# Optimization experiments

Hardware: AMD Instinct MI355X
Metric: run time of the kernel (lower is better)

## Reference

```python
import jax, jax.numpy as jnp
import numpy as np

N = 200000      # nodes (1000 graphs x 200 nodes)
E = 1600000     # edges
N1 = 100000     # nodes after pool 1
E2 = 100000     # edges of pooled graph
N2 = 50000      # nodes after pool 2
B = 1000        # graphs
F_IN, C1, C2, H, NCLS = 1, 32, 64, 25, 10


def setup_inputs() -> dict:
    key = jax.random.key(0)
    ks = jax.random.split(key, 16)
    def lin(k, i, o):
        return jax.random.normal(k, (i, o), jnp.float32) / np.sqrt(i)
    inp = {
        'x': jax.random.normal(ks[0], (N, F_IN), jnp.float32),
        'pos': jax.random.uniform(ks[1], (N, 2), jnp.float32),
        'edge_index': jax.random.randint(ks[2], (2, E), 0, N, dtype=jnp.int32),
        'edge_attr': jax.random.uniform(ks[3], (E, 2), jnp.float32),
        'batch': (jnp.arange(N, dtype=jnp.int32) // (N // B)),
        'cluster1': (jnp.arange(N, dtype=jnp.int32) // 2),      # pairs of consecutive nodes -> same graph
        'edge_index2': jax.random.randint(ks[4], (2, E2), 0, N1, dtype=jnp.int32),
        'cluster2': (jnp.arange(N1, dtype=jnp.int32) // 2),
        'n1_w1': lin(ks[5], 2, H), 'n1_b1': jnp.zeros((H,), jnp.float32),
        'n1_w2': lin(ks[6], H, F_IN * C1), 'n1_b2': jnp.zeros((F_IN * C1,), jnp.float32),
        'root1': lin(ks[7], F_IN, C1), 'bias1': jnp.zeros((C1,), jnp.float32),
        'n2_w1': lin(ks[8], 2, H), 'n2_b1': jnp.zeros((H,), jnp.float32),
        'n2_w2': lin(ks[9], H, C1 * C2), 'n2_b2': jnp.zeros((C1 * C2,), jnp.float32),
        'root2': lin(ks[10], C1, C2), 'bias2': jnp.zeros((C2,), jnp.float32),
        'fc1_w': lin(ks[11], C2, 128), 'fc1_b': jnp.zeros((128,), jnp.float32),
        'fc2_w': lin(ks[12], 128, NCLS), 'fc2_b': jnp.zeros((NCLS,), jnp.float32),
    }
    return inp


def _cartesian(ei, pos):
    # PyG transforms.Cartesian(norm=True, cat=False)
    cart = pos[ei[0]] - pos[ei[1]]                      # [E, 2]
    m = jnp.max(jnp.abs(cart))
    return cart / (2.0 * m) + 0.5


def _nnconv(x, ei, ea, w1, b1, w2, b2, root, bias, n_nodes, c_in, c_out):
    # edge-conditioned weights: MLP(edge_attr) -> [E, c_in, c_out]
    w = (jax.nn.relu(ea @ w1 + b1) @ w2 + b2).reshape(-1, c_in, c_out)
    msg = jnp.einsum('ei,eio->eo', x[ei[0]], w)          # per-edge matmul with gathered src feats
    agg = jax.ops.segment_sum(msg, ei[1], num_segments=n_nodes)
    return agg + x @ root + bias


def _segment_mean(v, seg, n):
    s = jax.ops.segment_sum(v, seg, num_segments=n)
    c = jax.ops.segment_sum(jnp.ones((v.shape[0], 1), v.dtype), seg, num_segments=n)
    return s / jnp.maximum(c, 1.0)


def reference(x, pos, edge_index, edge_attr, batch, cluster1, edge_index2, cluster2,
              n1_w1, n1_b1, n1_w2, n1_b2, root1, bias1,
              n2_w1, n2_b1, n2_w2, n2_b2, root2, bias2,
              fc1_w, fc1_b, fc2_w, fc2_b):
    h = jax.nn.elu(_nnconv(x, edge_index, edge_attr, n1_w1, n1_b1, n1_w2, n1_b2,
                           root1, bias1, N, F_IN, C1))
    # max_pool(cluster1): segment-max feats, mean pos, carry batch; recompute Cartesian attrs
    x1 = jax.ops.segment_max(h, cluster1, num_segments=N1)
    pos1 = _segment_mean(pos, cluster1, N1)
    batch1 = jax.ops.segment_max(batch, cluster1, num_segments=N1)
    ea2 = _cartesian(edge_index2, pos1)
    h2 = jax.nn.elu(_nnconv(x1, edge_index2, ea2, n2_w1, n2_b1, n2_w2, n2_b2,
                            root2, bias2, N1, C1, C2))
    # max_pool_x(cluster2)
    x2 = jax.ops.segment_max(h2, cluster2, num_segments=N2)
    batch2 = jax.ops.segment_max(batch1, cluster2, num_segments=N2)
    g = _segment_mean(x2, batch2, B)                    # global_mean_pool -> [B, 64]
    z = jax.nn.elu(g @ fc1_w + fc1_b)                   # dropout is identity in eval
    return jax.nn.log_softmax(z @ fc2_w + fc2_b, axis=1)
```

## Files before the change

kernel.cpp:

```cpp
#include <hip/hip_runtime.h>
#include <hip/hip_bf16.h>

#define N_NODES 200000
#define E1 1600000
#define N1P 100000
#define E2P 100000
#define N2P 50000
#define BGR 1000
#define C1 32
#define C2 64
#define HIDN 25
#define NCLS 10

typedef short short8 __attribute__((ext_vector_type(8)));
typedef int int4v __attribute__((ext_vector_type(4)));
typedef float f32x4 __attribute__((ext_vector_type(4)));
typedef float f32x2 __attribute__((ext_vector_type(2)));

union FragU { int4v i; short8 s; };

__device__ __forceinline__ float elu1(float v) {
    return v > 0.f ? v : expm1f(v);
}
__device__ __forceinline__ float bf2f(unsigned short u) {
    return __uint_as_float(((unsigned int)u) << 16);
}
__device__ __forceinline__ unsigned int pk_bf16(float a, float b) {
    unsigned int r;
    asm("v_cvt_pk_bf16_f32 %0, %1, %2" : "=v"(r) : "v"(a), "v"(b));
    return r;
}
__device__ __forceinline__ void atomic_pk_bf16(unsigned short* p, unsigned int pk) {
    asm volatile("global_atomic_pk_add_bf16 %0, %1, off" :: "v"(p), "v"(pk) : "memory");
}

__global__ __launch_bounds__(256) void bgbuild_kernel(
    const float* __restrict__ w2a, const float* __restrict__ b2a,
    const float* __restrict__ w2b, const float* __restrict__ b2b,
    unsigned int* __restrict__ W2f, unsigned int* __restrict__ Bg)
{
    int blk = blockIdx.x, t = threadIdx.x;
    if (blk < 2) {
        int q = blk * 256 + t;
        int jj = q & 3, l = (q >> 2) & 63, m = q >> 8;
        int k0 = (l >> 4) * 8 + 2 * jj;
        int o = 2 * (l & 15) + m;
        float v0 = (k0 < 25) ? w2a[k0 * 32 + o] : (k0 == 25 ? b2a[o] : 0.f);
        int k1 = k0 + 1;
        float v1 = (k1 < 25) ? w2a[k1 * 32 + o] : (k1 == 25 ? b2a[o] : 0.f);
        W2f[q] = pk_bf16(v0, v1);
    } else {
        int idx = (blk - 2) * 256 + t;
        if (idx >= 26 * 4 * 64 * 4) return;
        int g0 = idx * 2;
        int j = g0 & 7;
        int l = (g0 >> 3) & 63;
        int nb = (g0 >> 9) & 3;
        int kt = g0 >> 11;
        int k = kt * 32 + (l >> 4) * 8 + j;
        int o = (nb >> 1) * 32 + 2 * (l & 15) + (nb & 1);
        float v0, v1;
        if (k < 800) { v0 = w2b[k * 64 + o]; v1 = w2b[(k + 1) * 64 + o]; }
        else         { v0 = b2b[(k - 800) * 64 + o]; v1 = b2b[(k - 799) * 64 + o]; }
        Bg[idx] = pk_bf16(v0, v1);
    }
}

__global__ __launch_bounds__(256) void conv1_kernel(
    const float* __restrict__ x, const float* __restrict__ ea,
    const int* __restrict__ ei,
    const float* __restrict__ w1, const float* __restrict__ b1,
    const unsigned int* __restrict__ W2f,
    unsigned short* __restrict__ agg1b)
{
    __shared__ unsigned int afrag[16][4][64];
    __shared__ int dst_lds[256];

    int t = threadIdx.x;
    int e = blockIdx.x * 256 + t;
    f32x2 a = ((const f32x2*)ea)[e];
    int s = ei[e], d = ei[E1 + e];
    float xv = x[s];
    dst_lds[t] = d;

    float v[26];
#pragma unroll
    for (int h = 0; h < HIDN; ++h) {
        float u = fmaf(a.x, w1[h], fmaf(a.y, w1[HIDN + h], b1[h]));
        v[h] = fmaxf(u, 0.f) * xv;
    }
    v[25] = xv;

    int tile = t >> 4, r16 = t & 15;
#pragma unroll
    for (int p = 0; p < 13; ++p) {
        int g = p >> 2, j = p & 3;
        afrag[tile][j][g * 16 + r16] = pk_bf16(v[2 * p], v[2 * p + 1]);
    }
    afrag[tile][1][48 + r16] = 0;
    afrag[tile][2][48 + r16] = 0;
    afrag[tile][3][48 + r16] = 0;
    __syncthreads();

    int lane = t & 63, wave = t >> 6;
    FragU bf0, bf1;
    bf0.i = *(const int4v*)(W2f + lane * 4);
    bf1.i = *(const int4v*)(W2f + (64 + lane) * 4);
    int c = lane & 15, rg = lane >> 4;

#pragma unroll
    for (int ti = 0; ti < 4; ++ti) {
        int tl = wave * 4 + ti;
        FragU af;
        af.i.x = afrag[tl][0][lane];
        af.i.y = afrag[tl][1][lane];
        af.i.z = afrag[tl][2][lane];
        af.i.w = afrag[tl][3][lane];
        f32x4 a0 = (f32x4){0.f, 0.f, 0.f, 0.f};
        f32x4 a1 = (f32x4){0.f, 0.f, 0.f, 0.f};
        a0 = __builtin_amdgcn_mfma_f32_16x16x32_bf16(af.s, bf0.s, a0, 0, 0, 0);
        a1 = __builtin_amdgcn_mfma_f32_16x16x32_bf16(af.s, bf1.s, a1, 0, 0, 0);
#pragma unroll
        for (int jj = 0; jj < 4; ++jj) {
            int le = tl * 16 + rg * 4 + jj;
            atomic_pk_bf16(agg1b + (size_t)dst_lds[le] * C1 + 2 * c,
                           pk_bf16(a0[jj], a1[jj]));
        }
    }
}

__global__ __launch_bounds__(256) void pool1_kernel(
    const unsigned short* __restrict__ agg1b, const float* __restrict__ x,
    const float* __restrict__ root1, const float* __restrict__ bias1,
    const float* __restrict__ pos, unsigned short* __restrict__ x1b,
    float* __restrict__ pos1)
{
    int t = blockIdx.x * blockDim.x + threadIdx.x;
    if (t >= N1P * C1) return;
    int j = t >> 5, o = t & 31;
    int na = 2 * j, nb = 2 * j + 1;
    float r = root1[o], bo = bias1[o];
    float ha = elu1(bf2f(agg1b[(size_t)na * C1 + o]) + x[na] * r + bo);
    float hb = elu1(bf2f(agg1b[(size_t)nb * C1 + o]) + x[nb] * r + bo);
    float mx = fmaxf(ha, hb);
    x1b[t] = (unsigned short)(pk_bf16(mx, mx) & 0xffffu);
    if (o < 2) pos1[j * 2 + o] = 0.5f * (pos[na * 2 + o] + pos[nb * 2 + o]);
}

__global__ __launch_bounds__(256) void maxabs_kernel(
    const int* __restrict__ ei2, const float* __restrict__ pos1,
    unsigned int* __restrict__ maxbits)
{
    int e = blockIdx.x * blockDim.x + threadIdx.x;
    float m = 0.f;
    if (e < E2P) {
        int s = ei2[e], d = ei2[E2P + e];
        float c0 = pos1[2 * s] - pos1[2 * d];
        float c1 = pos1[2 * s + 1] - pos1[2 * d + 1];
        m = fmaxf(fabsf(c0), fabsf(c1));
    }
#pragma unroll
    for (int off = 32; off; off >>= 1)
        m = fmaxf(m, __shfl_down(m, off));
    if ((threadIdx.x & 63) == 0)
        atomicMax(maxbits, __float_as_uint(m));
}

__global__ __launch_bounds__(256) void conv2_kernel(
    const int* __restrict__ ei2, const float* __restrict__ pos1,
    const unsigned short* __restrict__ x1b,
    const float* __restrict__ w1, const float* __restrict__ b1,
    const unsigned int* __restrict__ maxbits,
    const unsigned int* __restrict__ Bg,
    unsigned short* __restrict__ agg2b)
{
    __shared__ __align__(16) unsigned short xs_lds[128][40];
    __shared__ unsigned int hidb[128][14];
    __shared__ int dst_lds[128];

    int t = threadIdx.x;
    int base = blockIdx.x * 128;

    if (t < 128) {
        int ge = base + t;
        bool ok = ge < E2P;
        float inv = 0.5f / __uint_as_float(maxbits[0]);
        int s = 0, d = 0;
        if (ok) { s = ei2[ge]; d = ei2[E2P + ge]; }
        dst_lds[t] = d;
        float a0 = (pos1[2 * s] - pos1[2 * d]) * inv + 0.5f;
        float a1 = (pos1[2 * s + 1] - pos1[2 * d + 1]) * inv + 0.5f;
        float hv[26];
#pragma unroll
        for (int h = 0; h < HIDN; ++h) {
            float u = fmaf(a0, w1[h], fmaf(a1, w1[HIDN + h], b1[h]));
            hv[h] = ok ? fmaxf(u, 0.f) : 0.f;
        }
        hv[25] = 0.f;
#pragma unroll
        for (int p = 0; p < 13; ++p)
            hidb[t][p] = pk_bf16(hv[2 * p], hv[2 * p + 1]);
        const int4v* xp = (const int4v*)(x1b + (size_t)s * C1);
#pragma unroll
        for (int q = 0; q < 4; ++q) {
            int4v z4 = (int4v){0, 0, 0, 0};
            *(int4v*)&xs_lds[t][q * 8] = ok ? xp[q] : z4;
        }
    }
    __syncthreads();

    int lane = t & 63, wave = t >> 6;
    int c = lane & 15, rg = lane >> 4;

    FragU xv2[2];
    float xfl[2][8];
#pragma unroll
    for (int ti = 0; ti < 2; ++ti) {
        int row = (wave * 2 + ti) * 16 + c;
        xv2[ti].i = *(const int4v*)&xs_lds[row][rg * 8];
#pragma unroll
        for (int g2 = 0; g2 < 4; ++g2) {
            unsigned int u = (unsigned int)xv2[ti].i[g2];
            xfl[ti][2 * g2]     = __uint_as_float(u << 16);
            xfl[ti][2 * g2 + 1] = __uint_as_float(u & 0xffff0000u);
        }
    }

    f32x4 acc[2][4];
#pragma unroll
    for (int ti = 0; ti < 2; ++ti)
#pragma unroll
        for (int nb = 0; nb < 4; ++nb)
            acc[ti][nb] = (f32x4){0.f, 0.f, 0.f, 0.f};

    const int4v* Bg4 = (const int4v*)Bg;
    FragU bf[4];
#pragma unroll
    for (int nb = 0; nb < 4; ++nb)
        bf[nb].i = Bg4[nb * 64 + lane];

#pragma unroll
    for (int kt = 0; kt < 25; ++kt) {
        FragU bn[4];
#pragma unroll
        for (int nb = 0; nb < 4; ++nb)
            bn[nb].i = Bg4[((kt + 1) * 4 + nb) * 64 + lane];
#pragma unroll
        for (int ti = 0; ti < 2; ++ti) {
            unsigned int hu = hidb[(wave * 2 + ti) * 16 + c][kt >> 1];
            float hvv = bf2f((unsigned short)((kt & 1) ? (hu >> 16) : (hu & 0xffffu)));
            FragU af;
            af.i.x = pk_bf16(hvv * xfl[ti][0], hvv * xfl[ti][1]);
            af.i.y = pk_bf16(hvv * xfl[ti][2], hvv * xfl[ti][3]);
            af.i.z = pk_bf16(hvv * xfl[ti][4], hvv * xfl[ti][5]);
            af.i.w = pk_bf16(hvv * xfl[ti][6], hvv * xfl[ti][7]);
#pragma unroll
            for (int nb = 0; nb < 4; ++nb)
                acc[ti][nb] = __builtin_amdgcn_mfma_f32_16x16x32_bf16(af.s, bf[nb].s, acc[ti][nb], 0, 0, 0);
        }
#pragma unroll
        for (int nb = 0; nb < 4; ++nb) bf[nb] = bn[nb];
    }
#pragma unroll
    for (int ti = 0; ti < 2; ++ti)
#pragma unroll
        for (int nb = 0; nb < 4; ++nb)
            acc[ti][nb] = __builtin_amdgcn_mfma_f32_16x16x32_bf16(xv2[ti].s, bf[nb].s, acc[ti][nb], 0, 0, 0);

#pragma unroll
    for (int ti = 0; ti < 2; ++ti) {
        int tl = wave * 2 + ti;
#pragma unroll
        for (int jj = 0; jj < 4; ++jj) {
            int le = tl * 16 + rg * 4 + jj;
            if (base + le < E2P) {
                unsigned short* dp = agg2b + (size_t)dst_lds[le] * C2;
                atomic_pk_bf16(dp + 2 * c,      pk_bf16(acc[ti][0][jj], acc[ti][1][jj]));
                atomic_pk_bf16(dp + 32 + 2 * c, pk_bf16(acc[ti][2][jj], acc[ti][3][jj]));
            }
        }
    }
}

__global__ __launch_bounds__(256) void pool2_head_kernel(
    const unsigned short* __restrict__ agg2b, const unsigned short* __restrict__ x1b,
    const float* __restrict__ root2, const float* __restrict__ bias2,
    const float* __restrict__ fc1w, const float* __restrict__ fc1b,
    const float* __restrict__ fc2w, const float* __restrict__ fc2b,
    float* __restrict__ out)
{
    int b = blockIdx.x;
    int t = threadIdx.x;
    int w = t >> 6, o = t & 63;
    __shared__ float part[4][C2];
    __shared__ float gs[C2];
    __shared__ float zs[128];
    __shared__ float ls[NCLS];

    float r2[C1];
#pragma unroll
    for (int i = 0; i < C1; ++i) r2[i] = root2[i * C2 + o];
    float bo = bias2[o];

    float sum = 0.f;
    for (int jj = w; jj < 50; jj += 4) {
        int j = b * 50 + jj;
        float hv[2];
#pragma unroll
        for (int tt = 0; tt < 2; ++tt) {
            int n = 2 * j + tt;
            float a = bf2f(agg2b[(size_t)n * C2 + o]) + bo;
            const int4v* xp = (const int4v*)(x1b + (size_t)n * C1);
#pragma unroll
            for (int q = 0; q < 4; ++q) {
                int4v v4 = xp[q];
#pragma unroll
                for (int g2 = 0; g2 < 4; ++g2) {
                    unsigned int u = (unsigned int)v4[g2];
                    a = fmaf(__uint_as_float(u << 16),         r2[q * 8 + 2 * g2],     a);
                    a = fmaf(__uint_as_float(u & 0xffff0000u), r2[q * 8 + 2 * g2 + 1], a);
                }
            }
            hv[tt] = elu1(a);
        }
        sum += fmaxf(hv[0], hv[1]);
    }
    part[w][o] = sum;
    __syncthreads();
    if (w == 0)
        gs[o] = (part[0][o] + part[1][o] + part[2][o] + part[3][o]) * (1.f / 50.f);
    __syncthreads();
    if (t < 128) {
        float z = fc1b[t];
#pragma unroll
        for (int i = 0; i < C2; ++i) z = fmaf(gs[i], fc1w[i * 128 + t], z);
        zs[t] = elu1(z);
    }
    __syncthreads();
    if (t < NCLS) {
        float l = fc2b[t];
#pragma unroll
        for (int k = 0; k < 128; ++k) l = fmaf(zs[k], fc2w[k * NCLS + t], l);
        ls[t] = l;
    }
    __syncthreads();
    if (t < NCLS) {
        float mx = ls[0];
#pragma unroll
        for (int cc = 1; cc < NCLS; ++cc) mx = fmaxf(mx, ls[cc]);
        float se = 0.f;
#pragma unroll
        for (int cc = 0; cc < NCLS; ++cc) se += expf(ls[cc] - mx);
        out[b * NCLS + t] = ls[t] - mx - logf(se);
    }
}

extern "C" void kernel_launch(void* const* d_in, const int* in_sizes, int n_in,
                              void* d_out, int out_size, void* d_ws, size_t ws_size,
                              hipStream_t stream)
{
    const float* x    = (const float*)d_in[0];
    const float* pos  = (const float*)d_in[1];
    const int*   ei   = (const int*)d_in[2];
    const float* ea   = (const float*)d_in[3];
    const int*   ei2  = (const int*)d_in[6];
    const float* n1w1 = (const float*)d_in[8];
    const float* n1b1 = (const float*)d_in[9];
    const float* n1w2 = (const float*)d_in[10];
    const float* n1b2 = (const float*)d_in[11];
    const float* root1= (const float*)d_in[12];
    const float* bias1= (const float*)d_in[13];
    const float* n2w1 = (const float*)d_in[14];
    const float* n2b1 = (const float*)d_in[15];
    const float* n2w2 = (const float*)d_in[16];
    const float* n2b2 = (const float*)d_in[17];
    const float* root2= (const float*)d_in[18];
    const float* bias2= (const float*)d_in[19];
    const float* fc1w = (const float*)d_in[20];
    const float* fc1b = (const float*)d_in[21];
    const float* fc2w = (const float*)d_in[22];
    const float* fc2b = (const float*)d_in[23];
    float* out = (float*)d_out;

    char* w = (char*)d_ws;
    unsigned short* agg1b = (unsigned short*)w;  w += (size_t)N_NODES * C1 * 2;
    unsigned short* x1b   = (unsigned short*)w;  w += (size_t)N1P * C1 * 2;
    float* pos1 = (float*)w;                     w += (size_t)N1P * 2 * 4;
    unsigned int* maxbits = (unsigned int*)w;    w += 256;
    unsigned short* agg2b = (unsigned short*)w;  w += (size_t)N1P * C2 * 2;
    unsigned int* Bg = (unsigned int*)w;         w += 26624 * 4;
    unsigned int* W2f = (unsigned int*)w;        w += 512 * 4;

    hipMemsetAsync(agg1b, 0, (size_t)N_NODES * C1 * 2, stream);
    hipMemsetAsync(agg2b, 0, (size_t)N1P * C2 * 2, stream);
    hipMemsetAsync(maxbits, 0, 256, stream);

    bgbuild_kernel<<<106, 256, 0, stream>>>(n1w2, n1b2, n2w2, n2b2, W2f, Bg);
    conv1_kernel<<<E1 / 256, 256, 0, stream>>>(x, ea, ei, n1w1, n1b1, W2f, agg1b);
    pool1_kernel<<<(N1P * C1 + 255) / 256, 256, 0, stream>>>(agg1b, x, root1, bias1, pos, x1b, pos1);
    maxabs_kernel<<<(E2P + 255) / 256, 256, 0, stream>>>(ei2, pos1, maxbits);
    conv2_kernel<<<(E2P + 127) / 128, 256, 0, stream>>>(ei2, pos1, x1b, n2w1, n2b1, maxbits, Bg, agg2b);
    pool2_head_kernel<<<BGR, 256, 0, stream>>>(agg2b, x1b, root2, bias2,
                                               fc1w, fc1b, fc2w, fc2b, out);
}
```

Measured before the change: 186.6 us.

## Fold pooled-position max reduction into weight-prep kernel and merge memsets

Removes the separate maxabs kernel and the pos1 buffer. Pooled positions are recomputed on the fly from the original pos array, inside the weight-prep kernel for the max-abs reduction and in conv2 for the edge attributes. The three memsets are merged into one contiguous zeroing by reordering the workspace layout. This saves one kernel launch, two memset calls and the pos1 round trip, at the cost of an extra gather per edge endpoint and a grid-stride loop in the small prep kernel.

```diff
diff --git a/kernel.cpp b/kernel.cpp
--- a/kernel.cpp
+++ b/kernel.cpp
@@ -37,7 +37,9 @@
 __global__ __launch_bounds__(256) void bgbuild_kernel(
     const float* __restrict__ w2a, const float* __restrict__ b2a,
     const float* __restrict__ w2b, const float* __restrict__ b2b,
-    unsigned int* __restrict__ W2f, unsigned int* __restrict__ Bg)
+    const float* __restrict__ pos, const int* __restrict__ ei2,
+    unsigned int* __restrict__ W2f, unsigned int* __restrict__ Bg,
+    unsigned int* __restrict__ maxbits)
 {
     int blk = blockIdx.x, t = threadIdx.x;
     if (blk < 2) {
@@ -51,19 +53,34 @@
         W2f[q] = pk_bf16(v0, v1);
     } else {
         int idx = (blk - 2) * 256 + t;
-        if (idx >= 26 * 4 * 64 * 4) return;
-        int g0 = idx * 2;
-        int j = g0 & 7;
-        int l = (g0 >> 3) & 63;
-        int nb = (g0 >> 9) & 3;
-        int kt = g0 >> 11;
-        int k = kt * 32 + (l >> 4) * 8 + j;
-        int o = (nb >> 1) * 32 + 2 * (l & 15) + (nb & 1);
-        float v0, v1;
-        if (k < 800) { v0 = w2b[k * 64 + o]; v1 = w2b[(k + 1) * 64 + o]; }
-        else         { v0 = b2b[(k - 800) * 64 + o]; v1 = b2b[(k - 799) * 64 + o]; }
-        Bg[idx] = pk_bf16(v0, v1);
-    }
+        if (idx < 26 * 4 * 64 * 4) {
+            int g0 = idx * 2;
+            int j = g0 & 7;
+            int l = (g0 >> 3) & 63;
+            int nb = (g0 >> 9) & 3;
+            int kt = g0 >> 11;
+            int k = kt * 32 + (l >> 4) * 8 + j;
+            int o = (nb >> 1) * 32 + 2 * (l & 15) + (nb & 1);
+            float v0, v1;
+            if (k < 800) { v0 = w2b[k * 64 + o]; v1 = w2b[(k + 1) * 64 + o]; }
+            else         { v0 = b2b[(k - 800) * 64 + o]; v1 = b2b[(k - 799) * 64 + o]; }
+            Bg[idx] = pk_bf16(v0, v1);
+        }
+    }
+    float m = 0.f;
+    for (int e = blk * 256 + t; e < E2P; e += gridDim.x * 256) {
+        int s = ei2[e], d = ei2[E2P + e];
+        f32x2 ps0 = ((const f32x2*)pos)[2 * s], ps1 = ((const f32x2*)pos)[2 * s + 1];
+        f32x2 pd0 = ((const f32x2*)pos)[2 * d], pd1 = ((const f32x2*)pos)[2 * d + 1];
+        float c0 = 0.5f * (ps0.x + ps1.x) - 0.5f * (pd0.x + pd1.x);
+        float c1 = 0.5f * (ps0.y + ps1.y) - 0.5f * (pd0.y + pd1.y);
+        m = fmaxf(m, fmaxf(fabsf(c0), fabsf(c1)));
+    }
+#pragma unroll
+    for (int off = 32; off; off >>= 1)
+        m = fmaxf(m, __shfl_down(m, off));
+    if ((t & 63) == 0)
+        atomicMax(maxbits, __float_as_uint(m));
 }
 
 __global__ __launch_bounds__(256) void conv1_kernel(
@@ -132,8 +149,7 @@
 __global__ __launch_bounds__(256) void pool1_kernel(
     const unsigned short* __restrict__ agg1b, const float* __restrict__ x,
     const float* __restrict__ root1, const float* __restrict__ bias1,
-    const float* __restrict__ pos, unsigned short* __restrict__ x1b,
-    float* __restrict__ pos1)
+    unsigned short* __restrict__ x1b)
 {
     int t = blockIdx.x * blockDim.x + threadIdx.x;
     if (t >= N1P * C1) return;
@@ -144,30 +160,10 @@
     float hb = elu1(bf2f(agg1b[(size_t)nb * C1 + o]) + x[nb] * r + bo);
     float mx = fmaxf(ha, hb);
     x1b[t] = (unsigned short)(pk_bf16(mx, mx) & 0xffffu);
-    if (o < 2) pos1[j * 2 + o] = 0.5f * (pos[na * 2 + o] + pos[nb * 2 + o]);
-}
-
-__global__ __launch_bounds__(256) void maxabs_kernel(
-    const int* __restrict__ ei2, const float* __restrict__ pos1,
-    unsigned int* __restrict__ maxbits)
-{
-    int e = blockIdx.x * blockDim.x + threadIdx.x;
-    float m = 0.f;
-    if (e < E2P) {
-        int s = ei2[e], d = ei2[E2P + e];
-        float c0 = pos1[2 * s] - pos1[2 * d];
-        float c1 = pos1[2 * s + 1] - pos1[2 * d + 1];
-        m = fmaxf(fabsf(c0), fabsf(c1));
-    }
-#pragma unroll
-    for (int off = 32; off; off >>= 1)
-        m = fmaxf(m, __shfl_down(m, off));
-    if ((threadIdx.x & 63) == 0)
-        atomicMax(maxbits, __float_as_uint(m));
 }
 
 __global__ __launch_bounds__(256) void conv2_kernel(
-    const int* __restrict__ ei2, const float* __restrict__ pos1,
+    const int* __restrict__ ei2, const float* __restrict__ pos,
     const unsigned short* __restrict__ x1b,
     const float* __restrict__ w1, const float* __restrict__ b1,
     const unsigned int* __restrict__ maxbits,
@@ -188,8 +184,10 @@
         int s = 0, d = 0;
         if (ok) { s = ei2[ge]; d = ei2[E2P + ge]; }
         dst_lds[t] = d;
-        float a0 = (pos1[2 * s] - pos1[2 * d]) * inv + 0.5f;
-        float a1 = (pos1[2 * s + 1] - pos1[2 * d + 1]) * inv + 0.5f;
+        f32x2 ps0 = ((const f32x2*)pos)[2 * s], ps1 = ((const f32x2*)pos)[2 * s + 1];
+        f32x2 pd0 = ((const f32x2*)pos)[2 * d], pd1 = ((const f32x2*)pos)[2 * d + 1];
+        float a0 = (0.5f * (ps0.x + ps1.x) - 0.5f * (pd0.x + pd1.x)) * inv + 0.5f;
+        float a1 = (0.5f * (ps0.y + ps1.y) - 0.5f * (pd0.y + pd1.y)) * inv + 0.5f;
         float hv[26];
 #pragma unroll
         for (int h = 0; h < HIDN; ++h) {
@@ -384,22 +382,20 @@
 
     char* w = (char*)d_ws;
     unsigned short* agg1b = (unsigned short*)w;  w += (size_t)N_NODES * C1 * 2;
+    unsigned short* agg2b = (unsigned short*)w;  w += (size_t)N1P * C2 * 2;
+    unsigned int* maxbits = (unsigned int*)w;    w += 1024;
+    size_t zero_bytes = (size_t)N_NODES * C1 * 2 + (size_t)N1P * C2 * 2 + 1024;
     unsigned short* x1b   = (unsigned short*)w;  w += (size_t)N1P * C1 * 2;
-    float* pos1 = (float*)w;                     w += (size_t)N1P * 2 * 4;
-    unsigned int* maxbits = (unsigned int*)w;    w += 256;
-    unsigned short* agg2b = (unsigned short*)w;  w += (size_t)N1P * C2 * 2;
     unsigned int* Bg = (unsigned int*)w;         w += 26624 * 4;
     unsigned int* W2f = (unsigned int*)w;        w += 512 * 4;
 
-    hipMemsetAsync(agg1b, 0, (size_t)N_NODES * C1 * 2, stream);
-    hipMemsetAsync(agg2b, 0, (size_t)N1P * C2 * 2, stream);
-    hipMemsetAsync(maxbits, 0, 256, stream);
-
-    bgbuild_kernel<<<106, 256, 0, stream>>>(n1w2, n1b2, n2w2, n2b2, W2f, Bg);
+    hipMemsetAsync(agg1b, 0, zero_bytes, stream);
+
+    bgbuild_kernel<<<106, 256, 0, stream>>>(n1w2, n1b2, n2w2, n2b2, pos, ei2,
+                                            W2f, Bg, maxbits);
     conv1_kernel<<<E1 / 256, 256, 0, stream>>>(x, ea, ei, n1w1, n1b1, W2f, agg1b);
-    pool1_kernel<<<(N1P * C1 + 255) / 256, 256, 0, stream>>>(agg1b, x, root1, bias1, pos, x1b, pos1);
-    maxabs_kernel<<<(E2P + 255) / 256, 256, 0, stream>>>(ei2, pos1, maxbits);
-    conv2_kernel<<<(E2P + 127) / 128, 256, 0, stream>>>(ei2, pos1, x1b, n2w1, n2b1, maxbits, Bg, agg2b);
+    pool1_kernel<<<(N1P * C1 + 255) / 256, 256, 0, stream>>>(agg1b, x, root1, bias1, x1b);
+    conv2_kernel<<<(E2P + 127) / 128, 256, 0, stream>>>(ei2, pos, x1b, n2w1, n2b1, maxbits, Bg, agg2b);
     pool2_head_kernel<<<BGR, 256, 0, stream>>>(agg2b, x1b, root2, bias2,
                                                fc1w, fc1b, fc2w, fc2b, out);
 }
```

New measurement: 165.3 us. 11.4% less time.
